# Performance work log

Measured on AMD Instinct MI355X. Metric: run time of the kernel, lower is better.

The kernel has to match this reference:

```python
import jax, jax.numpy as jnp
import numpy as np

HIDDEN = 2048
NUM_HEADS = 8
NUM_KV_HEADS = 1
HEAD_DIM = 256
ROPE_THETA = 10000.0
T = 2048  # num tokens (single causal prefill sequence)
Q_SIZE = NUM_HEADS * HEAD_DIM        # 2048
KV_SIZE = NUM_KV_HEADS * HEAD_DIM    # 256


def _apply_rope(x, positions):
    # x: [T, n_heads, head_dim], neox style (rotate halves)
    half = HEAD_DIM // 2
    inv_freq = 1.0 / (ROPE_THETA ** (jnp.arange(half, dtype=jnp.float32) * 2.0 / HEAD_DIM))
    ang = positions.astype(jnp.float32)[:, None] * inv_freq[None, :]   # [T, half]
    cos = jnp.cos(ang)[:, None, :]
    sin = jnp.sin(ang)[:, None, :]
    x1, x2 = jnp.split(x, 2, axis=-1)
    return jnp.concatenate([x1 * cos - x2 * sin, x2 * cos + x1 * sin], axis=-1)


def setup_inputs() -> dict:
    key = jax.random.key(0)
    k1, k2, k3 = jax.random.split(key, 3)
    hidden_states = jax.random.normal(k1, (T, HIDDEN), dtype=jnp.float32)
    Wqkv = jax.random.normal(k2, (Q_SIZE + 2 * KV_SIZE, HIDDEN), dtype=jnp.float32) * 0.02
    Wo = jax.random.normal(k3, (HIDDEN, Q_SIZE), dtype=jnp.float32) * 0.02
    positions = jnp.arange(T, dtype=jnp.int32)
    return {"positions": positions, "hidden_states": hidden_states, "Wqkv": Wqkv, "Wo": Wo}


def reference(positions, hidden_states, Wqkv, Wo):
    scaling = HEAD_DIM ** -0.5
    qkv = hidden_states @ Wqkv.T                                   # [T, Q+2KV]
    q = qkv[:, :Q_SIZE].reshape(T, NUM_HEADS, HEAD_DIM)
    k = qkv[:, Q_SIZE:Q_SIZE + KV_SIZE].reshape(T, NUM_KV_HEADS, HEAD_DIM)
    v = qkv[:, Q_SIZE + KV_SIZE:].reshape(T, NUM_KV_HEADS, HEAD_DIM)
    q = _apply_rope(q, positions)
    k = _apply_rope(k, positions)
    # GQA: group query heads over kv heads
    g = NUM_HEADS // NUM_KV_HEADS
    qg = q.reshape(T, NUM_KV_HEADS, g, HEAD_DIM)
    scores = jnp.einsum('qhgd,khd->hgqk', qg, k) * scaling         # [kv, g, T, T]
    causal = jnp.arange(T)[:, None] >= jnp.arange(T)[None, :]
    scores = jnp.where(causal[None, None], scores, jnp.finfo(scores.dtype).min)
    probs = jax.nn.softmax(scores, axis=-1)
    attn = jnp.einsum('hgqk,khd->qhgd', probs, v).reshape(T, Q_SIZE)
    return attn @ Wo.T
```

## Files before the change

kernel.cpp:

```cpp
#include <hip/hip_runtime.h>
#include <hip/hip_bf16.h>

typedef __bf16 bf16x8 __attribute__((ext_vector_type(8)));
typedef __bf16 bf16x4 __attribute__((ext_vector_type(4)));
typedef float floatx4 __attribute__((ext_vector_type(4)));

#define QKV_SLICE 5242880
#define OUT_SLICE 4194304

__device__ __forceinline__ float fast_exp2(float x) {
    return __builtin_amdgcn_exp2f(x);
}

__device__ __forceinline__ void lds_barrier() {
    asm volatile("s_waitcnt lgkmcnt(0)\n\ts_barrier" ::: "memory");
}

__device__ __forceinline__ void gload16(const __bf16* g, __bf16* l) {
    __builtin_amdgcn_global_load_lds((const __attribute__((address_space(1))) void*)g,
                                     (__attribute__((address_space(3))) void*)l, 16, 0, 0);
}

__global__ __launch_bounds__(256) void cast_all(const float* __restrict__ hid,
                                                const float* __restrict__ wqkv,
                                                const float* __restrict__ wo,
                                                __bf16* __restrict__ Ah,
                                                __bf16* __restrict__ Wqkvh,
                                                __bf16* __restrict__ Woh) {
    const int n1 = 1048576, n2 = 1310720;
    int i = blockIdx.x * 256 + threadIdx.x;
    const float* in;
    __bf16* out;
    int j;
    if (i < n1) { in = hid; out = Ah; j = i; }
    else if (i < n1 + n2) { in = wqkv; out = Wqkvh; j = i - n1; }
    else { in = wo; out = Woh; j = i - n1 - n2; }
    float4 v = ((const float4*)in)[j];
    bf16x4 o;
    o[0] = (__bf16)v.x; o[1] = (__bf16)v.y; o[2] = (__bf16)v.z; o[3] = (__bf16)v.w;
    ((bf16x4*)out)[j] = o;
}

__global__ __launch_bounds__(256) void gemm_bt_splitk(const __bf16* __restrict__ A,
                                                      const __bf16* __restrict__ B,
                                                      __bf16* __restrict__ C,
                                                      int M, int N, int K) {
    __shared__ __attribute__((aligned(16))) __bf16 As[128 * 64];
    __shared__ __attribute__((aligned(16))) __bf16 Bs[128 * 64];

    int tid = threadIdx.x, lane = tid & 63, w = tid >> 6;
    int wm = (w >> 1) * 64, wn = (w & 1) * 64;
    int bm0 = blockIdx.x * 128, bn0 = blockIdx.y * 128;
    int r = lane & 15, q4 = lane >> 4;
    int rr = lane >> 2, qq = lane & 3;
    int Ksl = K / (int)gridDim.z;
    int kbase = (int)blockIdx.z * Ksl;

    const __bf16* Agp[4];
    const __bf16* Bgp[4];
    __bf16* Asd[4];
    __bf16* Bsd[4];
#pragma unroll
    for (int j = 0; j < 4; j++) {
        int c = w * 4 + j;
        int kk = c >> 3, g = c & 7;
        Agp[j] = A + (size_t)(bm0 + g * 16 + rr) * K + kbase + kk * 32 + qq * 8;
        Bgp[j] = B + (size_t)(bn0 + g * 16 + rr) * K + kbase + kk * 32 + qq * 8;
        Asd[j] = &As[c * 512];
        Bsd[j] = &Bs[c * 512];
    }

    floatx4 acc[4][4];
#pragma unroll
    for (int i = 0; i < 4; i++)
#pragma unroll
        for (int j = 0; j < 4; j++) acc[i][j] = (floatx4)0.f;

    for (int k0 = 0; k0 < Ksl; k0 += 64) {
        asm volatile("s_barrier" ::: "memory");
#pragma unroll
        for (int j = 0; j < 4; j++) {
            gload16(Agp[j] + k0, Asd[j]);
            gload16(Bgp[j] + k0, Bsd[j]);
        }
        asm volatile("s_waitcnt vmcnt(0)\n\ts_barrier" ::: "memory");

#pragma unroll
        for (int kk = 0; kk < 2; kk++) {
            bf16x8 a[4], b[4];
#pragma unroll
            for (int mt = 0; mt < 4; mt++)
                a[mt] = *(const bf16x8*)&As[(kk * 8 + (wm >> 4) + mt) * 512 + r * 32 + q4 * 8];
#pragma unroll
            for (int nt = 0; nt < 4; nt++)
                b[nt] = *(const bf16x8*)&Bs[(kk * 8 + (wn >> 4) + nt) * 512 + r * 32 + q4 * 8];
#pragma unroll
            for (int mt = 0; mt < 4; mt++)
#pragma unroll
                for (int nt = 0; nt < 4; nt++)
                    acc[mt][nt] = __builtin_amdgcn_mfma_f32_16x16x32_bf16(a[mt], b[nt], acc[mt][nt], 0, 0, 0);
        }
    }

    __bf16* Cp = C + (size_t)blockIdx.z * M * N;
#pragma unroll
    for (int mt = 0; mt < 4; mt++)
#pragma unroll
        for (int nt = 0; nt < 4; nt++) {
            int row = bm0 + wm + mt * 16 + q4 * 4;
            int col = bn0 + wn + nt * 16 + r;
#pragma unroll
            for (int i = 0; i < 4; i++)
                Cp[(size_t)(row + i) * N + col] = (__bf16)acc[mt][nt][i];
        }
}

__global__ __launch_bounds__(256) void rope_vtrans(const __bf16* __restrict__ qp,
                                                   const int* __restrict__ positions,
                                                   __bf16* __restrict__ Qo,
                                                   __bf16* __restrict__ Ko,
                                                   __bf16* __restrict__ Vt) {
    __shared__ float tile[32][33];
    int b = blockIdx.x;
    if (b < 9216) {
        int idx = b * 256 + threadIdx.x;
        int i = idx & 127;
        int th = idx >> 7;
        int head = th % 9;
        int t = th / 9;
        float invf = expf(-(float)i * 0.07195578415606394f);
        float ang = (float)positions[t] * invf;
        float s = sinf(ang), c = cosf(ang);
        size_t off = (size_t)t * 2560 + (head < 8 ? head * 256 : 2048);
        float x1 = 0.f, x2 = 0.f;
#pragma unroll
        for (int sp = 0; sp < 4; sp++) {
            x1 += (float)qp[sp * QKV_SLICE + off + i];
            x2 += (float)qp[sp * QKV_SLICE + off + i + 128];
        }
        if (head < 8) {
            const float qs = 0.09016844f;
            __bf16* dst = Qo + (size_t)t * 2048 + head * 256;
            dst[i]       = (__bf16)((x1 * c - x2 * s) * qs);
            dst[i + 128] = (__bf16)((x2 * c + x1 * s) * qs);
        } else {
            int sw = (t & 7) << 3;
            __bf16* dst = Ko + (size_t)t * 256;
            dst[i ^ sw]         = (__bf16)(x1 * c - x2 * s);
            dst[(i + 128) ^ sw] = (__bf16)(x2 * c + x1 * s);
        }
    } else {
        int bb = b - 9216;
        int bt = bb & 63;
        int bc = bb >> 6;
        int tx = threadIdx.x & 31;
        int ty0 = threadIdx.x >> 5;
#pragma unroll
        for (int ty = ty0; ty < 32; ty += 8) {
            size_t gi = (size_t)(bt * 32 + ty) * 2560 + 2304 + bc * 32 + tx;
            float v = 0.f;
#pragma unroll
            for (int sp = 0; sp < 4; sp++) v += (float)qp[sp * QKV_SLICE + gi];
            tile[ty][tx] = v;
        }
        __syncthreads();
#pragma unroll
        for (int ty = ty0; ty < 32; ty += 8)
            Vt[(size_t)bt * 8192 + (bc * 2 + (ty >> 4)) * 512 + (ty & 15) * 8
               + (tx >> 3) * 128 + (tx & 7)] = (__bf16)tile[tx][ty];
    }
}

__global__ __launch_bounds__(256, 2) void attn_kernel(const __bf16* __restrict__ Q,
                                                      const __bf16* __restrict__ Kg,
                                                      const __bf16* __restrict__ Vt,
                                                      __bf16* __restrict__ Opart,
                                                      float2* __restrict__ Ml) {
    __shared__ __attribute__((aligned(16))) __bf16 Ks[2][32 * 256];
    __shared__ __attribute__((aligned(16))) __bf16 Vs[2][16 * 512];
    __shared__ __attribute__((aligned(16))) __bf16 Ps[4][32][40];

    int hg = blockIdx.x;
    int rs = 203 - (int)blockIdx.y;
    int k, base;
    if (rs < 12)       { k = 1; base = 0; }
    else if (rs < 36)  { k = 2; base = 12; }
    else if (rs < 72)  { k = 3; base = 36; }
    else if (rs < 120) { k = 4; base = 72; }
    else if (rs < 180) { k = 5; base = 120; }
    else               { k = 6; base = 180; }
    int idx = rs - base;
    int s = idx % k;
    int g = (k - 1) * 12 + idx / k;
    int slot = base + idx - s;

    int start = s * 384;
    int end = g * 32 + 32;
    if (end > start + 384) end = start + 384;
    int ntiles = (end - start) >> 5;

    int tid = threadIdx.x, lane = tid & 63, w = tid >> 6;
    int r = lane & 15, q4 = lane >> 4;
    int h = hg * 4 + w;
    int sw = (r & 7) << 3;

    bf16x8 qf[2][8];
#pragma unroll
    for (int qt = 0; qt < 2; qt++) {
        const __bf16* qrow = Q + (size_t)(g * 32 + qt * 16 + r) * 2048 + h * 256 + q4 * 8;
#pragma unroll
        for (int ks = 0; ks < 8; ks++) qf[qt][ks] = *(const bf16x8*)(qrow + ks * 32);
    }

    bf16x8 ones;
#pragma unroll
    for (int i = 0; i < 8; i++) ones[i] = (__bf16)1.0f;

    floatx4 acc[2][16];
#pragma unroll
    for (int qt = 0; qt < 2; qt++)
#pragma unroll
        for (int i = 0; i < 16; i++) acc[qt][i] = (floatx4)0.f;
    floatx4 acc_l[2];
    acc_l[0] = (floatx4)0.f; acc_l[1] = (floatx4)0.f;

    {
        const __bf16* kp = Kg + (size_t)start * 256 + tid * 8;
        const __bf16* vp = Vt + (size_t)(start >> 5) * 8192 + tid * 8;
        __bf16* kl = &Ks[0][tid * 8];
        __bf16* vl = &Vs[0][tid * 8];
#pragma unroll
        for (int j = 0; j < 4; j++) {
            gload16(kp + j * 2048, kl + j * 2048);
            gload16(vp + j * 2048, vl + j * 2048);
        }
    }

    for (int t = 0; t < ntiles; t++) {
        int cb = t & 1;
        int kt0 = start + t * 32;
        asm volatile("s_barrier" ::: "memory");
        if (t + 1 < ntiles) {
            int kt1 = kt0 + 32;
            const __bf16* kp = Kg + (size_t)kt1 * 256 + tid * 8;
            const __bf16* vp = Vt + (size_t)(kt1 >> 5) * 8192 + tid * 8;
            __bf16* kl = &Ks[cb ^ 1][tid * 8];
            __bf16* vl = &Vs[cb ^ 1][tid * 8];
#pragma unroll
            for (int j = 0; j < 4; j++) {
                gload16(kp + j * 2048, kl + j * 2048);
                gload16(vp + j * 2048, vl + j * 2048);
            }
            asm volatile("s_waitcnt vmcnt(8)\n\ts_barrier" ::: "memory");
        } else {
            asm volatile("s_waitcnt vmcnt(0)\n\ts_barrier" ::: "memory");
        }

        floatx4 sc[2][2];
        sc[0][0] = (floatx4)0.f; sc[0][1] = (floatx4)0.f;
        sc[1][0] = (floatx4)0.f; sc[1][1] = (floatx4)0.f;
#pragma unroll
        for (int ks = 0; ks < 8; ks++) {
#pragma unroll
            for (int nt = 0; nt < 2; nt++) {
                bf16x8 kf = *(const bf16x8*)&Ks[cb][(nt * 16 + r) * 256 + ((ks * 32 + q4 * 8) ^ sw)];
#pragma unroll
                for (int qt = 0; qt < 2; qt++)
                    sc[qt][nt] = __builtin_amdgcn_mfma_f32_16x16x32_bf16(qf[qt][ks], kf, sc[qt][nt], 0, 0, 0);
            }
        }
        if (kt0 + 31 > g * 32) {
#pragma unroll
            for (int qt = 0; qt < 2; qt++) {
                int qbase = g * 32 + qt * 16 + q4 * 4;
#pragma unroll
                for (int nt = 0; nt < 2; nt++) {
                    int kpos = kt0 + nt * 16 + r;
#pragma unroll
                    for (int i = 0; i < 4; i++)
                        if (kpos > qbase + i) sc[qt][nt][i] = -3e38f;
                }
            }
        }

#pragma unroll
        for (int qt = 0; qt < 2; qt++)
#pragma unroll
            for (int nt = 0; nt < 2; nt++)
#pragma unroll
                for (int i = 0; i < 4; i++)
                    Ps[w][qt * 16 + q4 * 4 + i][(nt * 16 + r) ^ (q4 << 3)] = (__bf16)fast_exp2(sc[qt][nt][i]);
        __builtin_amdgcn_wave_barrier();
        bf16x8 pf[2];
#pragma unroll
        for (int qt = 0; qt < 2; qt++)
            pf[qt] = *(const bf16x8*)&Ps[w][qt * 16 + r][(q4 * 8) ^ ((r >> 2) << 3)];
        __builtin_amdgcn_wave_barrier();

#pragma unroll
        for (int n16 = 0; n16 < 16; n16++) {
            bf16x8 vf = *(const bf16x8*)&Vs[cb][n16 * 512 + lane * 8];
            acc[0][n16] = __builtin_amdgcn_mfma_f32_16x16x32_bf16(pf[0], vf, acc[0][n16], 0, 0, 0);
            acc[1][n16] = __builtin_amdgcn_mfma_f32_16x16x32_bf16(pf[1], vf, acc[1][n16], 0, 0, 0);
        }
        acc_l[0] = __builtin_amdgcn_mfma_f32_16x16x32_bf16(pf[0], ones, acc_l[0], 0, 0, 0);
        acc_l[1] = __builtin_amdgcn_mfma_f32_16x16x32_bf16(pf[1], ones, acc_l[1], 0, 0, 0);
    }

    size_t base_row = (size_t)(slot + s) * 256 + hg * 128 + w * 32;
#pragma unroll
    for (int qt = 0; qt < 2; qt++)
#pragma unroll
        for (int n16 = 0; n16 < 16; n16++)
#pragma unroll
            for (int i = 0; i < 4; i++)
                Opart[(base_row + qt * 16 + q4 * 4 + i) * 256 + n16 * 16 + r] = (__bf16)acc[qt][n16][i];
    if (r == 0) {
#pragma unroll
        for (int qt = 0; qt < 2; qt++)
#pragma unroll
            for (int i = 0; i < 4; i++)
                Ml[base_row + qt * 16 + q4 * 4 + i] = make_float2(0.f, acc_l[qt][i]);
    }
}

__global__ __launch_bounds__(256) void combine_kernel(const __bf16* __restrict__ Opart,
                                                      const float2* __restrict__ Ml,
                                                      __bf16* __restrict__ attnb) {
    int wid = blockIdx.x * 4 + (threadIdx.x >> 6);
    int lane = threadIdx.x & 63;
    int t = wid >> 3, h = wid & 7;
    int g = t >> 5, r32 = t & 31;
    int qt = r32 >> 4, row16 = r32 & 15;
    int hg = h >> 2, w = h & 3;
    int k = g / 12 + 1;
    int fg = 6 * k * (k - 1) + (g - 12 * (k - 1)) * k;

    float ls[6];
    size_t rbase[6];
    for (int s = 0; s < k; s++) {
        rbase[s] = (size_t)(fg + s) * 256 + hg * 128 + w * 32 + qt * 16 + row16;
        ls[s] = Ml[rbase[s]].y;
    }
    float L = 0.f;
    float o[4] = {0.f, 0.f, 0.f, 0.f};
    for (int s = 0; s < k; s++) {
        L += ls[s];
        bf16x4 v = *(const bf16x4*)&Opart[rbase[s] * 256 + lane * 4];
#pragma unroll
        for (int j = 0; j < 4; j++) o[j] += (float)v[j];
    }
    float inv = 1.f / L;
    bf16x4 ov;
#pragma unroll
    for (int j = 0; j < 4; j++) ov[j] = (__bf16)(o[j] * inv);
    *(bf16x4*)&attnb[(size_t)t * 2048 + h * 256 + lane * 4] = ov;
}

__global__ __launch_bounds__(256) void add_out(const __bf16* __restrict__ p,
                                               float* __restrict__ out, int n4) {
    int i = blockIdx.x * 256 + threadIdx.x;
    if (i < n4) {
        float o[4] = {0.f, 0.f, 0.f, 0.f};
#pragma unroll
        for (int s = 0; s < 4; s++) {
            bf16x4 a = ((const bf16x4*)(p + (size_t)s * OUT_SLICE))[i];
#pragma unroll
            for (int j = 0; j < 4; j++) o[j] += (float)a[j];
        }
        float4 ov;
        ov.x = o[0]; ov.y = o[1]; ov.z = o[2]; ov.w = o[3];
        ((float4*)out)[i] = ov;
    }
}

extern "C" void kernel_launch(void* const* d_in, const int* in_sizes, int n_in,
                              void* d_out, int out_size, void* d_ws, size_t ws_size,
                              hipStream_t stream) {
    const int* positions = (const int*)d_in[0];
    const float* hidden  = (const float*)d_in[1];
    const float* Wqkv    = (const float*)d_in[2];
    const float* Wo      = (const float*)d_in[3];
    float* out = (float*)d_out;

    char* ws = (char*)d_ws;
    const size_t MB = 1024 * 1024;
    __bf16* Ah    = (__bf16*)(ws + 0 * MB);
    __bf16* Woh   = (__bf16*)(ws + 8 * MB);
    __bf16* Qb    = (__bf16*)(ws + 16 * MB);
    __bf16* Kb    = (__bf16*)(ws + 24 * MB);
    __bf16* Vtb   = (__bf16*)(ws + 25 * MB);
    __bf16* Wqkvh = (__bf16*)(ws + 26 * MB);
    __bf16* qkvp  = (__bf16*)(ws + 36 * MB);
    __bf16* Opart = (__bf16*)(ws + 26 * MB);
    float2* Ml    = (float2*)(ws + 52 * MB);
    __bf16* attnb = Ah;
    __bf16* gp    = (__bf16*)(ws + 26 * MB);

    cast_all<<<13312, 256, 0, stream>>>(hidden, Wqkv, Wo, Ah, Wqkvh, Woh);

    gemm_bt_splitk<<<dim3(16, 20, 4), 256, 0, stream>>>(Ah, Wqkvh, qkvp, 2048, 2560, 2048);

    rope_vtrans<<<9728, 256, 0, stream>>>(qkvp, positions, Qb, Kb, Vtb);

    attn_kernel<<<dim3(2, 204), 256, 0, stream>>>(Qb, Kb, Vtb, Opart, Ml);
    combine_kernel<<<4096, 256, 0, stream>>>(Opart, Ml, attnb);

    gemm_bt_splitk<<<dim3(16, 16, 4), 256, 0, stream>>>(attnb, Woh, gp, 2048, 2048, 2048);
    add_out<<<4096, 256, 0, stream>>>(gp, out, 1048576);
}
```

Before: 220.8 us.

## Fuse fp32-to-bf16 casts into GEMM loads with register prefetch and swizzled LDS

Removes the separate cast_all kernel. The GEMM now reads fp32 inputs directly, converts them to bf16 in registers, and prefetches the next k-tile into registers while the current tile is computed, storing into LDS with an XOR swizzle to avoid bank conflicts. Split-K drops from 4 to 2, which halves the partial-sum traffic in rope and add_out. Combine now writes fp32 attention output. The trade-offs are double the global read bytes per GEMM load, no async global-to-LDS copies, and fewer blocks for occupancy.

```diff
diff --git a/kernel.cpp b/kernel.cpp
--- a/kernel.cpp
+++ b/kernel.cpp
@@ -21,28 +21,17 @@
                                      (__attribute__((address_space(3))) void*)l, 16, 0, 0);
 }
 
-__global__ __launch_bounds__(256) void cast_all(const float* __restrict__ hid,
-                                                const float* __restrict__ wqkv,
-                                                const float* __restrict__ wo,
-                                                __bf16* __restrict__ Ah,
-                                                __bf16* __restrict__ Wqkvh,
-                                                __bf16* __restrict__ Woh) {
-    const int n1 = 1048576, n2 = 1310720;
-    int i = blockIdx.x * 256 + threadIdx.x;
-    const float* in;
-    __bf16* out;
-    int j;
-    if (i < n1) { in = hid; out = Ah; j = i; }
-    else if (i < n1 + n2) { in = wqkv; out = Wqkvh; j = i - n1; }
-    else { in = wo; out = Woh; j = i - n1 - n2; }
-    float4 v = ((const float4*)in)[j];
-    bf16x4 o;
-    o[0] = (__bf16)v.x; o[1] = (__bf16)v.y; o[2] = (__bf16)v.z; o[3] = (__bf16)v.w;
-    ((bf16x4*)out)[j] = o;
-}
-
-__global__ __launch_bounds__(256) void gemm_bt_splitk(const __bf16* __restrict__ A,
-                                                      const __bf16* __restrict__ B,
+__device__ __forceinline__ bf16x8 cvt8(const float* p) {
+    const float4* q = (const float4*)p;
+    float4 a = q[0], b = q[1];
+    bf16x8 v;
+    v[0] = (__bf16)a.x; v[1] = (__bf16)a.y; v[2] = (__bf16)a.z; v[3] = (__bf16)a.w;
+    v[4] = (__bf16)b.x; v[5] = (__bf16)b.y; v[6] = (__bf16)b.z; v[7] = (__bf16)b.w;
+    return v;
+}
+
+__global__ __launch_bounds__(256) void gemm_bt_splitk(const float* __restrict__ A,
+                                                      const float* __restrict__ B,
                                                       __bf16* __restrict__ C,
                                                       int M, int N, int K) {
     __shared__ __attribute__((aligned(16))) __bf16 As[128 * 64];
@@ -56,18 +45,19 @@
     int Ksl = K / (int)gridDim.z;
     int kbase = (int)blockIdx.z * Ksl;
 
-    const __bf16* Agp[4];
-    const __bf16* Bgp[4];
+    const float* Agp[4];
+    const float* Bgp[4];
     __bf16* Asd[4];
     __bf16* Bsd[4];
+    int wks = qq ^ ((rr >> 1) & 3);
 #pragma unroll
     for (int j = 0; j < 4; j++) {
         int c = w * 4 + j;
         int kk = c >> 3, g = c & 7;
         Agp[j] = A + (size_t)(bm0 + g * 16 + rr) * K + kbase + kk * 32 + qq * 8;
         Bgp[j] = B + (size_t)(bn0 + g * 16 + rr) * K + kbase + kk * 32 + qq * 8;
-        Asd[j] = &As[c * 512];
-        Bsd[j] = &Bs[c * 512];
+        Asd[j] = &As[c * 512 + rr * 32 + wks * 8];
+        Bsd[j] = &Bs[c * 512 + rr * 32 + wks * 8];
     }
 
     floatx4 acc[4][4];
@@ -76,24 +66,40 @@
 #pragma unroll
         for (int j = 0; j < 4; j++) acc[i][j] = (floatx4)0.f;
 
+    int kp = (q4 ^ ((r >> 1) & 3)) * 8;
+
+    bf16x8 ar[4], br[4];
+#pragma unroll
+    for (int j = 0; j < 4; j++) {
+        ar[j] = cvt8(Agp[j]);
+        br[j] = cvt8(Bgp[j]);
+    }
+
     for (int k0 = 0; k0 < Ksl; k0 += 64) {
-        asm volatile("s_barrier" ::: "memory");
+        lds_barrier();
 #pragma unroll
         for (int j = 0; j < 4; j++) {
-            gload16(Agp[j] + k0, Asd[j]);
-            gload16(Bgp[j] + k0, Bsd[j]);
-        }
-        asm volatile("s_waitcnt vmcnt(0)\n\ts_barrier" ::: "memory");
+            *(bf16x8*)Asd[j] = ar[j];
+            *(bf16x8*)Bsd[j] = br[j];
+        }
+        if (k0 + 64 < Ksl) {
+#pragma unroll
+            for (int j = 0; j < 4; j++) {
+                ar[j] = cvt8(Agp[j] + k0 + 64);
+                br[j] = cvt8(Bgp[j] + k0 + 64);
+            }
+        }
+        lds_barrier();
 
 #pragma unroll
         for (int kk = 0; kk < 2; kk++) {
             bf16x8 a[4], b[4];
 #pragma unroll
             for (int mt = 0; mt < 4; mt++)
-                a[mt] = *(const bf16x8*)&As[(kk * 8 + (wm >> 4) + mt) * 512 + r * 32 + q4 * 8];
+                a[mt] = *(const bf16x8*)&As[(kk * 8 + (wm >> 4) + mt) * 512 + r * 32 + kp];
 #pragma unroll
             for (int nt = 0; nt < 4; nt++)
-                b[nt] = *(const bf16x8*)&Bs[(kk * 8 + (wn >> 4) + nt) * 512 + r * 32 + q4 * 8];
+                b[nt] = *(const bf16x8*)&Bs[(kk * 8 + (wn >> 4) + nt) * 512 + r * 32 + kp];
 #pragma unroll
             for (int mt = 0; mt < 4; mt++)
 #pragma unroll
@@ -134,7 +140,7 @@
         size_t off = (size_t)t * 2560 + (head < 8 ? head * 256 : 2048);
         float x1 = 0.f, x2 = 0.f;
 #pragma unroll
-        for (int sp = 0; sp < 4; sp++) {
+        for (int sp = 0; sp < 2; sp++) {
             x1 += (float)qp[sp * QKV_SLICE + off + i];
             x2 += (float)qp[sp * QKV_SLICE + off + i + 128];
         }
@@ -160,7 +166,7 @@
             size_t gi = (size_t)(bt * 32 + ty) * 2560 + 2304 + bc * 32 + tx;
             float v = 0.f;
 #pragma unroll
-            for (int sp = 0; sp < 4; sp++) v += (float)qp[sp * QKV_SLICE + gi];
+            for (int sp = 0; sp < 2; sp++) v += (float)qp[sp * QKV_SLICE + gi];
             tile[ty][tx] = v;
         }
         __syncthreads();
@@ -326,7 +332,7 @@
 
 __global__ __launch_bounds__(256) void combine_kernel(const __bf16* __restrict__ Opart,
                                                       const float2* __restrict__ Ml,
-                                                      __bf16* __restrict__ attnb) {
+                                                      float* __restrict__ attnb) {
     int wid = blockIdx.x * 4 + (threadIdx.x >> 6);
     int lane = threadIdx.x & 63;
     int t = wid >> 3, h = wid & 7;
@@ -351,10 +357,9 @@
         for (int j = 0; j < 4; j++) o[j] += (float)v[j];
     }
     float inv = 1.f / L;
-    bf16x4 ov;
-#pragma unroll
-    for (int j = 0; j < 4; j++) ov[j] = (__bf16)(o[j] * inv);
-    *(bf16x4*)&attnb[(size_t)t * 2048 + h * 256 + lane * 4] = ov;
+    float4 ov;
+    ov.x = o[0] * inv; ov.y = o[1] * inv; ov.z = o[2] * inv; ov.w = o[3] * inv;
+    *(float4*)&attnb[(size_t)t * 2048 + h * 256 + lane * 4] = ov;
 }
 
 __global__ __launch_bounds__(256) void add_out(const __bf16* __restrict__ p,
@@ -363,7 +368,7 @@
     if (i < n4) {
         float o[4] = {0.f, 0.f, 0.f, 0.f};
 #pragma unroll
-        for (int s = 0; s < 4; s++) {
+        for (int s = 0; s < 2; s++) {
             bf16x4 a = ((const bf16x4*)(p + (size_t)s * OUT_SLICE))[i];
 #pragma unroll
             for (int j = 0; j < 4; j++) o[j] += (float)a[j];
@@ -385,27 +390,22 @@
 
     char* ws = (char*)d_ws;
     const size_t MB = 1024 * 1024;
-    __bf16* Ah    = (__bf16*)(ws + 0 * MB);
-    __bf16* Woh   = (__bf16*)(ws + 8 * MB);
-    __bf16* Qb    = (__bf16*)(ws + 16 * MB);
-    __bf16* Kb    = (__bf16*)(ws + 24 * MB);
-    __bf16* Vtb   = (__bf16*)(ws + 25 * MB);
-    __bf16* Wqkvh = (__bf16*)(ws + 26 * MB);
-    __bf16* qkvp  = (__bf16*)(ws + 36 * MB);
-    __bf16* Opart = (__bf16*)(ws + 26 * MB);
-    float2* Ml    = (float2*)(ws + 52 * MB);
-    __bf16* attnb = Ah;
-    __bf16* gp    = (__bf16*)(ws + 26 * MB);
-
-    cast_all<<<13312, 256, 0, stream>>>(hidden, Wqkv, Wo, Ah, Wqkvh, Woh);
-
-    gemm_bt_splitk<<<dim3(16, 20, 4), 256, 0, stream>>>(Ah, Wqkvh, qkvp, 2048, 2560, 2048);
+    float*  attnbf = (float*)(ws + 0 * MB);
+    __bf16* Qb     = (__bf16*)(ws + 17 * MB);
+    __bf16* Kb     = (__bf16*)(ws + 25 * MB);
+    __bf16* Vtb    = (__bf16*)(ws + 26 * MB);
+    __bf16* qkvp   = (__bf16*)(ws + 27 * MB);
+    __bf16* Opart  = (__bf16*)(ws + 48 * MB);
+    float2* Ml     = (float2*)(ws + 74 * MB);
+    __bf16* gp     = (__bf16*)(ws + 27 * MB);
+
+    gemm_bt_splitk<<<dim3(16, 20, 2), 256, 0, stream>>>(hidden, Wqkv, qkvp, 2048, 2560, 2048);
 
     rope_vtrans<<<9728, 256, 0, stream>>>(qkvp, positions, Qb, Kb, Vtb);
 
     attn_kernel<<<dim3(2, 204), 256, 0, stream>>>(Qb, Kb, Vtb, Opart, Ml);
-    combine_kernel<<<4096, 256, 0, stream>>>(Opart, Ml, attnb);
-
-    gemm_bt_splitk<<<dim3(16, 16, 4), 256, 0, stream>>>(attnb, Woh, gp, 2048, 2048, 2048);
+    combine_kernel<<<4096, 256, 0, stream>>>(Opart, Ml, attnbf);
+
+    gemm_bt_splitk<<<dim3(16, 16, 2), 256, 0, stream>>>(attnbf, Wo, gp, 2048, 2048, 2048);
     add_out<<<4096, 256, 0, stream>>>(gp, out, 1048576);
 }
```

New measurement: 246.6 us. 11.7% more time.

## Rewrite split-K GEMM with 256x256 tiles, double-buffered LDS and XOR swizzle

Applied to the files above, without the earlier changes.

Replaces the 128x128 split-K GEMM with a 512-thread kernel that computes 256x256 output tiles. It double-buffers the LDS staging so the next K-slice loads while the current one feeds MFMA, and XOR-swizzles the LDS layout to avoid bank conflicts. MFMA sections are also wrapped in s_setprio. The larger tiles raise data reuse, but they cut the grid to 320 and 256 blocks, use 128KB of LDS per block, and put 128 accumulator registers in each thread, which lowers occupancy.

```diff
diff --git a/kernel.cpp b/kernel.cpp
--- a/kernel.cpp
+++ b/kernel.cpp
@@ -10,10 +10,6 @@
 
 __device__ __forceinline__ float fast_exp2(float x) {
     return __builtin_amdgcn_exp2f(x);
-}
-
-__device__ __forceinline__ void lds_barrier() {
-    asm volatile("s_waitcnt lgkmcnt(0)\n\ts_barrier" ::: "memory");
 }
 
 __device__ __forceinline__ void gload16(const __bf16* g, __bf16* l) {
@@ -41,77 +37,87 @@
     ((bf16x4*)out)[j] = o;
 }
 
-__global__ __launch_bounds__(256) void gemm_bt_splitk(const __bf16* __restrict__ A,
-                                                      const __bf16* __restrict__ B,
-                                                      __bf16* __restrict__ C,
-                                                      int M, int N, int K) {
-    __shared__ __attribute__((aligned(16))) __bf16 As[128 * 64];
-    __shared__ __attribute__((aligned(16))) __bf16 Bs[128 * 64];
+__global__ __launch_bounds__(512) void gemm_bt_256(const __bf16* __restrict__ A,
+                                                   const __bf16* __restrict__ B,
+                                                   __bf16* __restrict__ C,
+                                                   int M, int N, int K) {
+    __shared__ __attribute__((aligned(16))) __bf16 As[2][256 * 64];
+    __shared__ __attribute__((aligned(16))) __bf16 Bs[2][256 * 64];
 
     int tid = threadIdx.x, lane = tid & 63, w = tid >> 6;
-    int wm = (w >> 1) * 64, wn = (w & 1) * 64;
-    int bm0 = blockIdx.x * 128, bn0 = blockIdx.y * 128;
+    int wm = w >> 2, wn = w & 3;
+    int bm0 = blockIdx.x * 256, bn0 = blockIdx.y * 256;
     int r = lane & 15, q4 = lane >> 4;
-    int rr = lane >> 2, qq = lane & 3;
     int Ksl = K / (int)gridDim.z;
     int kbase = (int)blockIdx.z * Ksl;
 
-    const __bf16* Agp[4];
-    const __bf16* Bgp[4];
-    __bf16* Asd[4];
-    __bf16* Bsd[4];
+    int srow = tid >> 3;
+    int sslot = (tid & 7) ^ (srow & 7);
+    const __bf16* Ag = A + (size_t)(bm0 + srow) * K + kbase + sslot * 8;
+    const __bf16* Bg = B + (size_t)(bn0 + srow) * K + kbase + sslot * 8;
+    size_t jstep = (size_t)64 * K;
+    __bf16* Ald = &As[0][0] + tid * 8;
+    __bf16* Bld = &Bs[0][0] + tid * 8;
+
+    floatx4 acc[8][4];
+#pragma unroll
+    for (int i = 0; i < 8; i++)
+#pragma unroll
+        for (int j = 0; j < 4; j++) acc[i][j] = (floatx4)0.f;
+
+    int nt = Ksl >> 6;
+
 #pragma unroll
     for (int j = 0; j < 4; j++) {
-        int c = w * 4 + j;
-        int kk = c >> 3, g = c & 7;
-        Agp[j] = A + (size_t)(bm0 + g * 16 + rr) * K + kbase + kk * 32 + qq * 8;
-        Bgp[j] = B + (size_t)(bn0 + g * 16 + rr) * K + kbase + kk * 32 + qq * 8;
-        Asd[j] = &As[c * 512];
-        Bsd[j] = &Bs[c * 512];
-    }
-
-    floatx4 acc[4][4];
-#pragma unroll
-    for (int i = 0; i < 4; i++)
-#pragma unroll
-        for (int j = 0; j < 4; j++) acc[i][j] = (floatx4)0.f;
-
-    for (int k0 = 0; k0 < Ksl; k0 += 64) {
-        asm volatile("s_barrier" ::: "memory");
-#pragma unroll
-        for (int j = 0; j < 4; j++) {
-            gload16(Agp[j] + k0, Asd[j]);
-            gload16(Bgp[j] + k0, Bsd[j]);
-        }
+        gload16(Ag + j * jstep, Ald + j * 4096);
+        gload16(Bg + j * jstep, Bld + j * 4096);
+    }
+
+    for (int t = 0; t < nt; t++) {
+        int cb = t & 1;
         asm volatile("s_waitcnt vmcnt(0)\n\ts_barrier" ::: "memory");
-
-#pragma unroll
-        for (int kk = 0; kk < 2; kk++) {
-            bf16x8 a[4], b[4];
-#pragma unroll
-            for (int mt = 0; mt < 4; mt++)
-                a[mt] = *(const bf16x8*)&As[(kk * 8 + (wm >> 4) + mt) * 512 + r * 32 + q4 * 8];
-#pragma unroll
-            for (int nt = 0; nt < 4; nt++)
-                b[nt] = *(const bf16x8*)&Bs[(kk * 8 + (wn >> 4) + nt) * 512 + r * 32 + q4 * 8];
-#pragma unroll
-            for (int mt = 0; mt < 4; mt++)
-#pragma unroll
-                for (int nt = 0; nt < 4; nt++)
-                    acc[mt][nt] = __builtin_amdgcn_mfma_f32_16x16x32_bf16(a[mt], b[nt], acc[mt][nt], 0, 0, 0);
+        if (t + 1 < nt) {
+            int ko = (t + 1) << 6;
+#pragma unroll
+            for (int j = 0; j < 4; j++) {
+                gload16(Ag + j * jstep + ko, Ald + (cb ^ 1) * 16384 + j * 4096);
+                gload16(Bg + j * jstep + ko, Bld + (cb ^ 1) * 16384 + j * 4096);
+            }
+        }
+
+#pragma unroll
+        for (int ks = 0; ks < 2; ks++) {
+            bf16x8 a[8], b[4];
+#pragma unroll
+            for (int m16 = 0; m16 < 8; m16++) {
+                int row = wm * 128 + m16 * 16 + r;
+                a[m16] = *(const bf16x8*)&As[cb][row * 64 + (((ks << 2) + q4) ^ (r & 7)) * 8];
+            }
+#pragma unroll
+            for (int n16 = 0; n16 < 4; n16++) {
+                int row = wn * 64 + n16 * 16 + r;
+                b[n16] = *(const bf16x8*)&Bs[cb][row * 64 + (((ks << 2) + q4) ^ (r & 7)) * 8];
+            }
+            __builtin_amdgcn_s_setprio(1);
+#pragma unroll
+            for (int m16 = 0; m16 < 8; m16++)
+#pragma unroll
+                for (int n16 = 0; n16 < 4; n16++)
+                    acc[m16][n16] = __builtin_amdgcn_mfma_f32_16x16x32_bf16(a[m16], b[n16], acc[m16][n16], 0, 0, 0);
+            __builtin_amdgcn_s_setprio(0);
         }
     }
 
     __bf16* Cp = C + (size_t)blockIdx.z * M * N;
 #pragma unroll
-    for (int mt = 0; mt < 4; mt++)
-#pragma unroll
-        for (int nt = 0; nt < 4; nt++) {
-            int row = bm0 + wm + mt * 16 + q4 * 4;
-            int col = bn0 + wn + nt * 16 + r;
+    for (int m16 = 0; m16 < 8; m16++)
+#pragma unroll
+        for (int n16 = 0; n16 < 4; n16++) {
+            int row = bm0 + wm * 128 + m16 * 16 + q4 * 4;
+            int col = bn0 + wn * 64 + n16 * 16 + r;
 #pragma unroll
             for (int i = 0; i < 4; i++)
-                Cp[(size_t)(row + i) * N + col] = (__bf16)acc[mt][nt][i];
+                Cp[(size_t)(row + i) * N + col] = (__bf16)acc[m16][n16][i];
         }
 }
 
@@ -399,13 +405,13 @@
 
     cast_all<<<13312, 256, 0, stream>>>(hidden, Wqkv, Wo, Ah, Wqkvh, Woh);
 
-    gemm_bt_splitk<<<dim3(16, 20, 4), 256, 0, stream>>>(Ah, Wqkvh, qkvp, 2048, 2560, 2048);
+    gemm_bt_256<<<dim3(8, 10, 4), 512, 0, stream>>>(Ah, Wqkvh, qkvp, 2048, 2560, 2048);
 
     rope_vtrans<<<9728, 256, 0, stream>>>(qkvp, positions, Qb, Kb, Vtb);
 
     attn_kernel<<<dim3(2, 204), 256, 0, stream>>>(Qb, Kb, Vtb, Opart, Ml);
     combine_kernel<<<4096, 256, 0, stream>>>(Opart, Ml, attnb);
 
-    gemm_bt_splitk<<<dim3(16, 16, 4), 256, 0, stream>>>(attnb, Woh, gp, 2048, 2048, 2048);
+    gemm_bt_256<<<dim3(8, 8, 4), 512, 0, stream>>>(attnb, Woh, gp, 2048, 2048, 2048);
     add_out<<<4096, 256, 0, stream>>>(gp, out, 1048576);
 }
```

Result: slower. 229.9 us (+4.1%).
